# Kernel optimization log

Measured on AMD Instinct MI355X. Metric: run time of the kernel, lower is better.

Reference implementation:

```python
import jax, jax.numpy as jnp
import numpy as np

L, B, C, OUT = 4, 4, 256, 4
H, W = 128, 128
HEADS, DH, G = 8, 32, 64
N = H * W
INNER = HEADS * DH
HID = 4 * C


def _ln(x, w, b, eps=1e-5):
    m = jnp.mean(x, -1, keepdims=True)
    v = jnp.mean((x - m) ** 2, -1, keepdims=True)
    return (x - m) / jnp.sqrt(v + eps) * w + b


def setup_inputs() -> dict:
    key = jax.random.key(0)
    ks = iter(jax.random.split(key, 16))
    nrm = lambda shape, s=0.02: jax.random.normal(next(ks), shape, jnp.float32) * s
    return dict(
        fx=jax.random.normal(next(ks), (B, N, C), jnp.float32),
        ln1_w=jnp.ones((L, C)), ln1_b=jnp.zeros((L, C)),
        convx_w=nrm((L, 3, 3, C, INNER)), convx_b=jnp.zeros((L, INNER)),
        convfx_w=nrm((L, 3, 3, C, INNER)), convfx_b=jnp.zeros((L, INNER)),
        slice_w=nrm((L, DH, G)), slice_b=jnp.zeros((L, G)),
        temperature=0.5 * jnp.ones((L, HEADS)),
        wq=nrm((L, DH, DH)), wk=nrm((L, DH, DH)), wv=nrm((L, DH, DH)),
        wo=nrm((L, INNER, C)), bo=jnp.zeros((L, C)),
        ln2_w=jnp.ones((L, C)), ln2_b=jnp.zeros((L, C)),
        w1=nrm((L, C, HID)), b1=jnp.zeros((L, HID)),
        w2=nrm((L, HID, C)), b2=jnp.zeros((L, C)),
        ln3_w=jnp.ones((C,)), ln3_b=jnp.zeros((C,)),
        w_out=nrm((C, OUT)), b_out=jnp.zeros((OUT,)),
    )


def reference(fx, ln1_w, ln1_b, convx_w, convx_b, convfx_w, convfx_b,
              slice_w, slice_b, temperature, wq, wk, wv, wo, bo,
              ln2_w, ln2_b, w1, b1, w2, b2, ln3_w, ln3_b, w_out, b_out):
    Bb = fx.shape[0]
    scale = DH ** -0.5
    for i in range(L):
        # --- Physics attention (slice attention) ---
        x = _ln(fx, ln1_w[i], ln1_b[i])
        ximg = x.reshape(Bb, H, W, C)  # NHWC
        conv = lambda w, b: jax.lax.conv_general_dilated(
            ximg, w, (1, 1), 'SAME',
            dimension_numbers=('NHWC', 'HWIO', 'NHWC')) + b
        fx_mid = conv(convfx_w[i], convfx_b[i]).reshape(Bb, N, HEADS, DH).transpose(0, 2, 1, 3)  # [B,h,N,d]
        x_mid = conv(convx_w[i], convx_b[i]).reshape(Bb, N, HEADS, DH).transpose(0, 2, 1, 3)
        temp = jnp.clip(temperature[i], 0.1, 5.0)[None, :, None, None]
        logits = (jnp.einsum('bhnd,dg->bhng', x_mid, slice_w[i]) + slice_b[i]) / temp
        sw = jax.nn.softmax(logits, axis=-1)  # [B,h,N,G]
        norm = sw.sum(2)  # [B,h,G]
        st = jnp.einsum('bhnc,bhng->bhgc', fx_mid, sw) / (norm + 1e-5)[..., None]  # [B,h,G,d]
        q = jnp.einsum('bhgc,cd->bhgd', st, wq[i])
        k = jnp.einsum('bhgc,cd->bhgd', st, wk[i])
        v = jnp.einsum('bhgc,cd->bhgd', st, wv[i])
        attn = jax.nn.softmax(jnp.einsum('bhgd,bhkd->bhgk', q, k) * scale, axis=-1)
        ot = jnp.einsum('bhgk,bhkd->bhgd', attn, v)  # [B,h,G,d]
        out_x = jnp.einsum('bhgc,bhng->bhnc', ot, sw)  # deslice back to points
        out_x = out_x.transpose(0, 2, 1, 3).reshape(Bb, N, INNER)
        fx = fx + out_x @ wo[i] + bo[i]
        # --- MLP (n_layers=0, no res inside) ---
        h = _ln(fx, ln2_w[i], ln2_b[i])
        h = jax.nn.gelu(h @ w1[i] + b1[i], approximate=False) @ w2[i] + b2[i]
        fx = fx + h
    # last-layer head
    return _ln(fx, ln3_w, ln3_b) @ w_out + b_out
```

## Files before the change

kernel.cpp:

```cpp
#include <hip/hip_runtime.h>
#include <hip/hip_bf16.h>

typedef __hip_bfloat16 bf16;
typedef __bf16 bfv8 __attribute__((ext_vector_type(8)));
typedef float f32x4 __attribute__((ext_vector_type(4)));

#define BB 4
#define HH 128
#define WWI 128
#define NN 16384
#define CC 256
#define LL 4
#define NHEADS 8
#define DHD 32
#define GG 64
#define INNERC 256
#define HIDD 1024
#define SPLIT 32
#define SSP 16

__device__ __forceinline__ float b2f(bf16 x) { return __bfloat162float(x); }
__device__ __forceinline__ bf16 f2b(float x) { return __float2bfloat16(x); }
__device__ __forceinline__ float us2f(unsigned short v) {
  return __uint_as_float(((unsigned)v) << 16);
}

__device__ __forceinline__ void async16(void* l, const void* g) {
  __builtin_amdgcn_global_load_lds(
      (const __attribute__((address_space(1))) void*)g,
      (__attribute__((address_space(3))) void*)l, 16, 0, 0);
}

__device__ __forceinline__ float wave_sum(float v) {
#pragma unroll
  for (int off = 32; off > 0; off >>= 1) v += __shfl_down(v, off, 64);
  return v;
}

__device__ __forceinline__ float gelu_exact(float x) {
  return 0.5f * x * (1.0f + erff(x * 0.70710678118654752f));
}

__global__ void transpose_cast_kernel(const float* __restrict__ src, bf16* __restrict__ dst,
                                      int R, int Cm) {
  __shared__ float tile[32][33];
  int tb = blockIdx.z;
  const float* s = src + (size_t)tb * R * Cm;
  bf16* d = dst + (size_t)tb * R * Cm;
  int c0 = blockIdx.x * 32, r0 = blockIdx.y * 32;
  int tx = threadIdx.x & 31, ty = threadIdx.x >> 5;
  for (int rr = ty; rr < 32; rr += 8) {
    int r = r0 + rr, c = c0 + tx;
    tile[rr][tx] = (r < R && c < Cm) ? s[(size_t)r * Cm + c] : 0.f;
  }
  __syncthreads();
  for (int cc = ty; cc < 32; cc += 8) {
    int c = c0 + cc, r = r0 + tx;
    if (c < Cm && r < R) d[(size_t)c * R + r] = f2b(tile[tx][cc]);
  }
}

__global__ void ln_kernel(const float* __restrict__ x, const float* __restrict__ w,
                          const float* __restrict__ b, bf16* __restrict__ out) {
  int pp = blockIdx.x;
  int t = threadIdx.x;
  float v = x[(size_t)pp * CC + t];
  float s = wave_sum(v);
  float sq = wave_sum(v * v);
  __shared__ float ls[4], lq[4];
  int wid = t >> 6, lane = t & 63;
  if (lane == 0) { ls[wid] = s; lq[wid] = sq; }
  __syncthreads();
  float tot = ls[0] + ls[1] + ls[2] + ls[3];
  float totq = lq[0] + lq[1] + lq[2] + lq[3];
  float mean = tot * (1.0f / CC);
  float var = totq * (1.0f / CC) - mean * mean;
  float rstd = rsqrtf(var + 1e-5f);
  float o = (v - mean) * rstd * w[t] + b[t];
  out[(size_t)pp * CC + t] = f2b(o);
}

__global__ __launch_bounds__(512) void conv_mfma_kernel(
    const bf16* __restrict__ xln, const bf16* __restrict__ wt,
    const float* __restrict__ bias, bf16* __restrict__ out,
    const float* __restrict__ zbuf) {
  __shared__ __align__(16) unsigned short As[3 * 130 * 64];
  __shared__ __align__(16) unsigned short Bsm[2][256 * 64];
  int bid = blockIdx.x;
  bid = (bid & 7) * 64 + (bid >> 3);
  int h = bid & 127;
  int b = bid >> 7;
  int t = threadIdx.x, lane = t & 63, wid = t >> 6;
  int wm = (wid & 1) * 64, wn = (wid >> 1) * 64;
  int l15 = lane & 15, l4 = lane >> 4;
  int wu = t & ~63;
  f32x4 acc[4][4];
#pragma unroll
  for (int mi = 0; mi < 4; ++mi)
#pragma unroll
    for (int ni = 0; ni < 4; ++ni) acc[mi][ni] = (f32x4){0.f, 0.f, 0.f, 0.f};
  const bf16* xbase = xln + (size_t)b * NN * CC;

  for (int q = 0; q < 4; ++q) {
#pragma unroll
    for (int k = 0; k < 6; ++k) {
      int u = t + k * 512;
      int jp = u & 7, pc = u >> 3;
      int r = pc / 130, cl = pc - r * 130;
      int j = jp ^ (cl & 7);
      int gr = h + r - 1, gc = cl - 1;
      const void* src =
          ((unsigned)gr < 128u && (unsigned)gc < 128u)
              ? (const void*)(xbase + ((size_t)(gr * WWI + gc)) * CC + q * 64 + j * 8)
              : (const void*)zbuf;
      async16(&As[(size_t)(wu + k * 512) * 8], src);
    }
    if (t < 48) {
      int u = t + 3072;
      int jp = u & 7, pc = u >> 3;
      int r = pc / 130, cl = pc - r * 130;
      int j = jp ^ (cl & 7);
      int gr = h + r - 1, gc = cl - 1;
      uint4 v = make_uint4(0u, 0u, 0u, 0u);
      if ((unsigned)gr < 128u && (unsigned)gc < 128u)
        v = *(const uint4*)(xbase + ((size_t)(gr * WWI + gc)) * CC + q * 64 + j * 8);
      *(uint4*)(&As[(size_t)u * 8]) = v;
    }
#pragma unroll
    for (int k = 0; k < 4; ++k) {
      int u = t + k * 512;
      int n = u >> 3, jp = u & 7, j = jp ^ (n & 7);
      async16(&Bsm[0][(size_t)(wu + k * 512) * 8],
              wt + (size_t)n * 256 + q * 64 + j * 8);
    }
    __syncthreads();

    for (int tap = 0; tap < 9; ++tap) {
      int cur = tap & 1;
      if (tap < 8) {
#pragma unroll
        for (int k = 0; k < 4; ++k) {
          int u = t + k * 512;
          int n = u >> 3, jp = u & 7, j = jp ^ (n & 7);
          async16(&Bsm[cur ^ 1][(size_t)(wu + k * 512) * 8],
                  wt + ((size_t)((tap + 1) * 256 + n)) * 256 + q * 64 + j * 8);
        }
      }
      int ky = tap / 3, kx = tap - ky * 3;
      const unsigned short* Bc = Bsm[cur];
#pragma unroll
      for (int s = 0; s < 2; ++s) {
        bfv8 af[4], bfr[4];
#pragma unroll
        for (int mi = 0; mi < 4; ++mi) {
          int cl = wm + mi * 16 + l15 + kx;
          af[mi] = *(const bfv8*)(&As[((size_t)(ky * 130 + cl)) * 64 +
                                      (((s * 4 + l4) ^ (cl & 7)) << 3)]);
        }
#pragma unroll
        for (int ni = 0; ni < 4; ++ni) {
          int rn = wn + ni * 16 + l15;
          bfr[ni] = *(const bfv8*)(&Bc[(size_t)rn * 64 + (((s * 4 + l4) ^ (rn & 7)) << 3)]);
        }
#pragma unroll
        for (int mi = 0; mi < 4; ++mi)
#pragma unroll
          for (int ni = 0; ni < 4; ++ni)
            acc[mi][ni] = __builtin_amdgcn_mfma_f32_16x16x32_bf16(af[mi], bfr[ni], acc[mi][ni], 0, 0, 0);
      }
      __syncthreads();
    }
  }
  int colB = wn + l15;
  int rowB = wm + l4 * 4;
#pragma unroll
  for (int ni = 0; ni < 4; ++ni) {
    int oc = colB + ni * 16;
    float bv = bias[oc];
#pragma unroll
    for (int mi = 0; mi < 4; ++mi) {
#pragma unroll
      for (int r = 0; r < 4; ++r) {
        int pix = rowB + mi * 16 + r;
        out[((size_t)(b * NN + h * WWI + pix)) * CC + oc] = f2b(acc[mi][ni][r] + bv);
      }
    }
  }
}

__global__ __launch_bounds__(256, 2) void gemm_acc_kernel(
    const bf16* __restrict__ A, const bf16* __restrict__ BT,
    const float* __restrict__ bias, float* __restrict__ outf,
    int M, int N, int K, size_t strideAz, size_t strideBz, size_t strideOz) {
  A  += (size_t)blockIdx.z * strideAz;
  BT += (size_t)blockIdx.z * strideBz;
  __shared__ __align__(16) unsigned short As[128 * 64];
  __shared__ __align__(16) unsigned short Bs[128 * 64];
  int m0 = blockIdx.x * 128, n0 = blockIdx.y * 128;
  int t = threadIdx.x, lane = t & 63, wid = t >> 6;
  int wm = (wid >> 1) * 64, wn = (wid & 1) * 64;
  int l15 = lane & 15, q4 = lane >> 4;
  int wg = wm >> 4, ng = wn >> 4;
  f32x4 acc[4][4];
#pragma unroll
  for (int mi = 0; mi < 4; ++mi)
#pragma unroll
    for (int ni = 0; ni < 4; ++ni) acc[mi][ni] = (f32x4){0.f, 0.f, 0.f, 0.f};

  for (int kb = 0; kb < K; kb += 64) {
    __syncthreads();
#pragma unroll
    for (int i = 0; i < 4; ++i) {
      int inst = wid * 4 + i;
      int g = inst >> 1, h2 = inst & 1;
      int row = g * 16 + l15;
      int kc = (h2 * 4 + q4) * 8;
      async16(&As[(size_t)g * 1024 + h2 * 512], A + (size_t)(m0 + row) * K + kb + kc);
      async16(&Bs[(size_t)g * 1024 + h2 * 512], BT + (size_t)(n0 + row) * K + kb + kc);
    }
    __syncthreads();
#pragma unroll
    for (int s = 0; s < 2; ++s) {
      int kgrp = s * 4 + q4;
      bfv8 af[4], bfr[4];
#pragma unroll
      for (int mi = 0; mi < 4; ++mi)
        af[mi] = *(const bfv8*)(&As[(size_t)(wg + mi) * 1024 + kgrp * 128 + l15 * 8]);
#pragma unroll
      for (int ni = 0; ni < 4; ++ni)
        bfr[ni] = *(const bfv8*)(&Bs[(size_t)(ng + ni) * 1024 + kgrp * 128 + l15 * 8]);
#pragma unroll
      for (int mi = 0; mi < 4; ++mi)
#pragma unroll
        for (int ni = 0; ni < 4; ++ni)
          acc[mi][ni] = __builtin_amdgcn_mfma_f32_16x16x32_bf16(af[mi], bfr[ni], acc[mi][ni], 0, 0, 0);
    }
  }
  int colB = n0 + wn + l15;
  int rowB = m0 + wm + q4 * 4;
#pragma unroll
  for (int ni = 0; ni < 4; ++ni) {
    int col = colB + ni * 16;
    float bv = bias[col];
#pragma unroll
    for (int mi = 0; mi < 4; ++mi) {
#pragma unroll
      for (int r = 0; r < 4; ++r) {
        int row = rowB + mi * 16 + r;
        outf[(size_t)blockIdx.z * strideOz + (size_t)row * N + col] += acc[mi][ni][r] + bv;
      }
    }
  }
}

__global__ __launch_bounds__(512) void mlp_fused_kernel(
    const bf16* __restrict__ xln, const bf16* __restrict__ w1t,
    const float* __restrict__ b1, const bf16* __restrict__ w2t,
    const float* __restrict__ b2, float* __restrict__ fx) {
  __shared__ __align__(16) unsigned short As[64 * 256];
  __shared__ __align__(16) bf16 Hs[64 * 128];
  __shared__ __align__(16) unsigned short Wb[128 * 256];
  int m0 = blockIdx.x * 64;
  int t = threadIdx.x, lane = t & 63, wid = t >> 6;
  int l15 = lane & 15, q4 = lane >> 4;
  int wm2 = (wid & 1) * 32, wn2 = (wid >> 1) * 32;
  int wm = (wid & 1) * 32, wn = (wid >> 1) * 64;
  int wu = t & ~63;

  const unsigned short* xg = (const unsigned short*)xln + (size_t)m0 * 256;
#pragma unroll
  for (int i = 0; i < 4; ++i) {
    int u = t + i * 512;
    int row = u >> 5;
    int su = (u & ~7) | ((u & 7) ^ (row & 7));
    async16(&As[(size_t)(wu + i * 512) * 8], xg + (size_t)su * 8);
  }
#pragma unroll
  for (int i = 0; i < 8; ++i) {
    int u = t + i * 512;
    int n = u >> 5, v = u & 31;
    int sv = (v & ~7) | ((v & 7) ^ (n & 7));
    async16(&Wb[(size_t)(wu + i * 512) * 8], w1t + (size_t)n * 256 + sv * 8);
  }

  f32x4 accO[2][4];
#pragma unroll
  for (int mi = 0; mi < 2; ++mi)
#pragma unroll
    for (int ni = 0; ni < 4; ++ni) accO[mi][ni] = (f32x4){0.f, 0.f, 0.f, 0.f};
  __syncthreads();

  for (int j = 0; j < 8; ++j) {
    int hbase = j * 128;
    f32x4 acc2[2][2];
#pragma unroll
    for (int mi = 0; mi < 2; ++mi)
#pragma unroll
      for (int nj = 0; nj < 2; ++nj) acc2[mi][nj] = (f32x4){0.f, 0.f, 0.f, 0.f};
#pragma unroll
    for (int kb = 0; kb < 4; ++kb) {
#pragma unroll
      for (int ks = 0; ks < 2; ++ks) {
        int kgrp = ks * 4 + q4;
        bfv8 af[2], bfr[2];
#pragma unroll
        for (int mi = 0; mi < 2; ++mi) {
          int row = wm2 + mi * 16 + l15;
          af[mi] = *(const bfv8*)(&As[row * 256 + kb * 64 + ((kgrp ^ (row & 7)) << 3)]);
        }
#pragma unroll
        for (int nj = 0; nj < 2; ++nj) {
          int n = wn2 + nj * 16 + l15;
          bfr[nj] = *(const bfv8*)(&Wb[n * 256 + kb * 64 + ((kgrp ^ (n & 7)) << 3)]);
        }
#pragma unroll
        for (int mi = 0; mi < 2; ++mi)
#pragma unroll
          for (int nj = 0; nj < 2; ++nj)
            acc2[mi][nj] = __builtin_amdgcn_mfma_f32_16x16x32_bf16(af[mi], bfr[nj], acc2[mi][nj], 0, 0, 0);
      }
    }
    __syncthreads();
#pragma unroll
    for (int i = 0; i < 8; ++i) {
      int u = t + i * 512;
      int n = u >> 4, v = u & 15;
      int sv = (v & ~7) | ((v & 7) ^ (n & 7));
      async16(&Wb[(size_t)(wu + i * 512) * 8], w2t + (size_t)n * 1024 + hbase + sv * 8);
    }
#pragma unroll
    for (int nj = 0; nj < 2; ++nj) {
      int coln = wn2 + nj * 16 + l15;
      float bv = b1[hbase + coln];
      int half = coln >> 6, sub = (coln >> 3) & 7, lo = coln & 7;
#pragma unroll
      for (int mi = 0; mi < 2; ++mi) {
#pragma unroll
        for (int r = 0; r < 4; ++r) {
          int row = wm2 + mi * 16 + q4 * 4 + r;
          float v = acc2[mi][nj][r] + bv;
          Hs[row * 128 + half * 64 + (((sub ^ (row & 7)) << 3) + lo)] = f2b(gelu_exact(v));
        }
      }
    }
    __syncthreads();
#pragma unroll
    for (int kb2 = 0; kb2 < 2; ++kb2) {
#pragma unroll
      for (int ks = 0; ks < 2; ++ks) {
        int kgrp = ks * 4 + q4;
        bfv8 af[2], bfr[4];
#pragma unroll
        for (int mi = 0; mi < 2; ++mi) {
          int row = wm + mi * 16 + l15;
          af[mi] = *(const bfv8*)(&Hs[row * 128 + kb2 * 64 + ((kgrp ^ (row & 7)) << 3)]);
        }
#pragma unroll
        for (int ni = 0; ni < 4; ++ni) {
          int n = wn + ni * 16 + l15;
          bfr[ni] = *(const bfv8*)(&Wb[n * 128 + kb2 * 64 + ((kgrp ^ (n & 7)) << 3)]);
        }
#pragma unroll
        for (int mi = 0; mi < 2; ++mi)
#pragma unroll
          for (int ni = 0; ni < 4; ++ni)
            accO[mi][ni] = __builtin_amdgcn_mfma_f32_16x16x32_bf16(af[mi], bfr[ni], accO[mi][ni], 0, 0, 0);
      }
    }
    if (j < 7) {
      __syncthreads();
#pragma unroll
      for (int i = 0; i < 8; ++i) {
        int u = t + i * 512;
        int n = u >> 5, v = u & 31;
        int sv = (v & ~7) | ((v & 7) ^ (n & 7));
        async16(&Wb[(size_t)(wu + i * 512) * 8],
                w1t + (size_t)(hbase + 128 + n) * 256 + sv * 8);
      }
      __syncthreads();
    }
  }
#pragma unroll
  for (int ni = 0; ni < 4; ++ni) {
    int col = wn + ni * 16 + l15;
    float bv = b2[col];
#pragma unroll
    for (int mi = 0; mi < 2; ++mi) {
#pragma unroll
      for (int r = 0; r < 4; ++r) {
        int row = m0 + wm + mi * 16 + q4 * 4 + r;
        fx[(size_t)row * 256 + col] += accO[mi][ni][r] + bv;
      }
    }
  }
}

__global__ __launch_bounds__(256) void slice_softmax_kernel(
    const bf16* __restrict__ xmid, const float* __restrict__ sw_w,
    const float* __restrict__ sw_b, const float* __restrict__ temp,
    bf16* __restrict__ swout) {
  __shared__ float wsm[32][64];
  __shared__ float xm[SSP][256];
  __shared__ float bias_s[64];
  __shared__ float rtc[8];
  int p0 = blockIdx.x * SSP;
  int t = threadIdx.x;
  for (int i = t; i < 2048; i += 256) wsm[i >> 6][i & 63] = sw_w[i];
  if (t < 64) bias_s[t] = sw_b[t];
  if (t < 8) {
    float x = temp[t];
    rtc[t] = 1.0f / fminf(fmaxf(x, 0.1f), 5.0f);
  }
  const unsigned short* xg = (const unsigned short*)xmid + (size_t)p0 * 256;
#pragma unroll
  for (int i2 = t; i2 < SSP * 32; i2 += 256) {
    uint4 v = ((const uint4*)xg)[i2];
    int p = i2 >> 5, c = (i2 & 31) << 3;
    xm[p][c + 0] = us2f((unsigned short)(v.x & 0xffff));
    xm[p][c + 1] = us2f((unsigned short)(v.x >> 16));
    xm[p][c + 2] = us2f((unsigned short)(v.y & 0xffff));
    xm[p][c + 3] = us2f((unsigned short)(v.y >> 16));
    xm[p][c + 4] = us2f((unsigned short)(v.z & 0xffff));
    xm[p][c + 5] = us2f((unsigned short)(v.z >> 16));
    xm[p][c + 6] = us2f((unsigned short)(v.w & 0xffff));
    xm[p][c + 7] = us2f((unsigned short)(v.w >> 16));
  }
  __syncthreads();
  int g = t & 63, pq = t >> 6;
  for (int pp2 = 0; pp2 < SSP / 4; ++pp2) {
    int p = pp2 * 4 + pq;
#pragma unroll
    for (int h = 0; h < NHEADS; ++h) {
      float acc = bias_s[g];
      const float* xr = &xm[p][h * 32];
#pragma unroll
      for (int d = 0; d < 32; ++d) acc += xr[d] * wsm[d][g];
      float logit = acc * rtc[h];
      float m = logit;
#pragma unroll
      for (int off = 32; off > 0; off >>= 1) m = fmaxf(m, __shfl_xor(m, off, 64));
      float e = __expf(logit - m);
      float s = e;
#pragma unroll
      for (int off = 32; off > 0; off >>= 1) s += __shfl_xor(s, off, 64);
      swout[(size_t)(p0 + p) * 512 + h * 64 + g] = f2b(e / s);
    }
  }
}

__global__ __launch_bounds__(256) void slice_st_kernel(
    const bf16* __restrict__ fxmid, const bf16* __restrict__ sw,
    float* __restrict__ stp, float* __restrict__ normp) {
  __shared__ __align__(16) unsigned short sw_s[64 * 64];
  __shared__ __align__(16) unsigned short fx_s[32 * 64];
  __shared__ float npart[2][64];
  int split = blockIdx.x, h = blockIdx.y, b = blockIdx.z;
  int t = threadIdx.x, w = t >> 6, lane = t & 63;
  int l15 = lane & 15, q4 = lane >> 4;
  int ns0 = split * (NN / SPLIT);
  const int NT = (NN / SPLIT) / 64;
  f32x4 acc0 = {0.f, 0.f, 0.f, 0.f}, acc1 = {0.f, 0.f, 0.f, 0.f};
  float nacc = 0.f;
  const unsigned short* swg = (const unsigned short*)sw + (size_t)b * NN * 512 + h * 64;
  const unsigned short* fxg = (const unsigned short*)fxmid + (size_t)b * NN * 256 + h * 32;

  for (int kt = 0; kt < NT; ++kt) {
    int n0 = ns0 + kt * 64;
    __syncthreads();
    if (w < 2) {
      int g = lane;
#pragma unroll
      for (int i = 0; i < 4; ++i) {
        int j = w + 2 * i;
        const unsigned short* p = swg + (size_t)(n0 + j * 8) * 512 + g;
        unsigned short v0 = p[0],     v1 = p[512],  v2 = p[1024], v3 = p[1536];
        unsigned short v4 = p[2048],  v5 = p[2560], v6 = p[3072], v7 = p[3584];
        nacc += us2f(v0) + us2f(v1) + us2f(v2) + us2f(v3) +
                us2f(v4) + us2f(v5) + us2f(v6) + us2f(v7);
        uint4 pk = make_uint4((unsigned)v0 | ((unsigned)v1 << 16),
                              (unsigned)v2 | ((unsigned)v3 << 16),
                              (unsigned)v4 | ((unsigned)v5 << 16),
                              (unsigned)v6 | ((unsigned)v7 << 16));
        ((uint4*)sw_s)[g * 8 + (j ^ (g & 7))] = pk;
      }
    } else {
      int d = lane & 31, nh = lane >> 5, w3 = w - 2;
#pragma unroll
      for (int i = 0; i < 2; ++i) {
        int nbase = (w3 * 2 + i) * 16 + nh * 8;
        const unsigned short* p = fxg + (size_t)(n0 + nbase) * 256 + d;
        unsigned short v0 = p[0],    v1 = p[256],  v2 = p[512],  v3 = p[768];
        unsigned short v4 = p[1024], v5 = p[1280], v6 = p[1536], v7 = p[1792];
        uint4 pk = make_uint4((unsigned)v0 | ((unsigned)v1 << 16),
                              (unsigned)v2 | ((unsigned)v3 << 16),
                              (unsigned)v4 | ((unsigned)v5 << 16),
                              (unsigned)v6 | ((unsigned)v7 << 16));
        int u = nbase >> 3;
        ((uint4*)fx_s)[d * 8 + (u ^ (d & 7))] = pk;
      }
    }
    __syncthreads();
    int gg = w * 16 + l15;
    int d0 = l15, d1 = 16 + l15;
#pragma unroll
    for (int ks = 0; ks < 2; ++ks) {
      bfv8 af  = ((const bfv8*)sw_s)[gg * 8 + ((ks * 4 + q4) ^ (gg & 7))];
      bfv8 bf0 = ((const bfv8*)fx_s)[d0 * 8 + ((ks * 4 + q4) ^ (d0 & 7))];
      bfv8 bf1 = ((const bfv8*)fx_s)[d1 * 8 + ((ks * 4 + q4) ^ (d1 & 7))];
      acc0 = __builtin_amdgcn_mfma_f32_16x16x32_bf16(af, bf0, acc0, 0, 0, 0);
      acc1 = __builtin_amdgcn_mfma_f32_16x16x32_bf16(af, bf1, acc1, 0, 0, 0);
    }
  }
  if (w < 2) npart[w][lane] = nacc;
  __syncthreads();
  int bh = b * NHEADS + h;
  if (t < 64) normp[(size_t)split * (BB * NHEADS * GG) + bh * 64 + t] = npart[0][t] + npart[1][t];
  size_t base = ((size_t)split * (BB * NHEADS * GG) + bh * 64) * 32;
#pragma unroll
  for (int r = 0; r < 4; ++r) {
    int g = w * 16 + q4 * 4 + r;
    stp[base + (size_t)g * 32 + l15] = acc0[r];
    stp[base + (size_t)g * 32 + 16 + l15] = acc1[r];
  }
}

__global__ __launch_bounds__(256) void attn_kernel(
    const float* __restrict__ stp, const float* __restrict__ normp,
    const float* __restrict__ wq, const float* __restrict__ wk,
    const float* __restrict__ wv, float* __restrict__ ot) {
  __shared__ float wqs[32 * 32], wks[32 * 32], wvs[32 * 32];
  __shared__ float st[GG][DHD + 1];
  __shared__ float qq[GG][DHD + 1], kk[GG][DHD + 1], vv[GG][DHD + 1];
  __shared__ float pm[GG][GG + 1];
  __shared__ float nrm[GG];
  int bh = blockIdx.x;
  int t = threadIdx.x;
  ((float4*)wqs)[t] = ((const float4*)wq)[t];
  ((float4*)wks)[t] = ((const float4*)wk)[t];
  ((float4*)wvs)[t] = ((const float4*)wv)[t];
  if (t < 64) {
    float ns = 0.f;
    for (int s = 0; s < SPLIT; ++s) ns += normp[(size_t)s * (BB * NHEADS * GG) + bh * 64 + t];
    nrm[t] = 1.0f / (ns + 1e-5f);
  }
  __syncthreads();
#pragma unroll
  for (int i = 0; i < 8; ++i) {
    int idx = t + i * 256;
    int g = idx >> 5, d = idx & 31;
    float a = 0.f;
    for (int s = 0; s < SPLIT; ++s)
      a += stp[((size_t)s * (BB * NHEADS * GG) + bh * 64 + g) * 32 + d];
    st[g][d] = a * nrm[g];
  }
  __syncthreads();
#pragma unroll
  for (int i = 0; i < 8; ++i) {
    int idx = t + i * 256;
    int g = idx >> 5, d = idx & 31;
    float aq = 0.f, ak = 0.f, av = 0.f;
#pragma unroll
    for (int c = 0; c < 32; ++c) {
      float sv = st[g][c];
      aq += sv * wqs[c * 32 + d];
      ak += sv * wks[c * 32 + d];
      av += sv * wvs[c * 32 + d];
    }
    qq[g][d] = aq; kk[g][d] = ak; vv[g][d] = av;
  }
  __syncthreads();
  {
    int g = t >> 2, sub = t & 3;
    float sc[16];
    float m = -1e30f;
    const float scale = 0.17677669529663687f;
#pragma unroll
    for (int jj = 0; jj < 16; ++jj) {
      int j = sub * 16 + jj;
      float a = 0.f;
#pragma unroll
      for (int d = 0; d < 32; ++d) a += qq[g][d] * kk[j][d];
      a *= scale;
      sc[jj] = a;
      m = fmaxf(m, a);
    }
    m = fmaxf(m, __shfl_xor(m, 1, 64));
    m = fmaxf(m, __shfl_xor(m, 2, 64));
    float ssum = 0.f;
#pragma unroll
    for (int jj = 0; jj < 16; ++jj) { sc[jj] = __expf(sc[jj] - m); ssum += sc[jj]; }
    ssum += __shfl_xor(ssum, 1, 64);
    ssum += __shfl_xor(ssum, 2, 64);
    float rs = 1.0f / ssum;
#pragma unroll
    for (int jj = 0; jj < 16; ++jj) pm[g][sub * 16 + jj] = sc[jj] * rs;
  }
  __syncthreads();
#pragma unroll
  for (int i = 0; i < 8; ++i) {
    int idx = t + i * 256;
    int g = idx >> 5, d = idx & 31;
    float a = 0.f;
#pragma unroll
    for (int j = 0; j < GG; ++j) a += pm[g][j] * vv[j][d];
    ot[((size_t)bh * GG + g) * DHD + d] = a;
  }
}

__global__ __launch_bounds__(256) void wc_kernel(const float* __restrict__ ot,
                                                 const float* __restrict__ wo,
                                                 bf16* __restrict__ wct) {
  __shared__ float ots[GG][DHD];
  int bh = blockIdx.x;
  int h = bh & 7, b = bh >> 3;
  int t = threadIdx.x;
  for (int i = t; i < GG * DHD; i += 256) ots[i >> 5][i & 31] = ot[(size_t)bh * (GG * DHD) + i];
  float wol[DHD];
#pragma unroll
  for (int d = 0; d < DHD; ++d) wol[d] = wo[(size_t)(h * DHD + d) * CC + t];
  __syncthreads();
  bf16* dst = wct + ((size_t)b * CC + t) * (NHEADS * GG) + h * GG;
#pragma unroll 4
  for (int g = 0; g < GG; ++g) {
    float a = 0.f;
#pragma unroll
    for (int d = 0; d < DHD; ++d) a += wol[d] * ots[g][d];
    dst[g] = f2b(a);
  }
}

__global__ void head_kernel(const float* __restrict__ fx, const float* __restrict__ w,
                            const float* __restrict__ b, const float* __restrict__ wout,
                            const float* __restrict__ bout, float* __restrict__ out) {
  int pp = blockIdx.x;
  int t = threadIdx.x;
  float v = fx[(size_t)pp * CC + t];
  float s = wave_sum(v);
  float sq = wave_sum(v * v);
  __shared__ float ls[4], lq[4];
  int wid = t >> 6, lane = t & 63;
  if (lane == 0) { ls[wid] = s; lq[wid] = sq; }
  __syncthreads();
  float tot = ls[0] + ls[1] + ls[2] + ls[3];
  float totq = lq[0] + lq[1] + lq[2] + lq[3];
  float mean = tot * (1.0f / CC);
  float var = totq * (1.0f / CC) - mean * mean;
  float rstd = rsqrtf(var + 1e-5f);
  float xn = (v - mean) * rstd * w[t] + b[t];
  __shared__ float xs[CC];
  xs[t] = xn;
  __syncthreads();
  if (t < 4) {
    float a = bout[t];
    for (int c = 0; c < CC; ++c) a += xs[c] * wout[c * 4 + t];
    out[(size_t)pp * 4 + t] = a;
  }
}

extern "C" void kernel_launch(void* const* d_in, const int* in_sizes, int n_in,
                              void* d_out, int out_size, void* d_ws, size_t ws_size,
                              hipStream_t stream) {
  const float* fx_in      = (const float*)d_in[0];
  const float* ln1_w      = (const float*)d_in[1];
  const float* ln1_b      = (const float*)d_in[2];
  const float* convx_w    = (const float*)d_in[3];
  const float* convx_b    = (const float*)d_in[4];
  const float* convfx_w   = (const float*)d_in[5];
  const float* convfx_b   = (const float*)d_in[6];
  const float* slice_w    = (const float*)d_in[7];
  const float* slice_b    = (const float*)d_in[8];
  const float* temperature= (const float*)d_in[9];
  const float* wq         = (const float*)d_in[10];
  const float* wk         = (const float*)d_in[11];
  const float* wv         = (const float*)d_in[12];
  const float* wo         = (const float*)d_in[13];
  const float* bo         = (const float*)d_in[14];
  const float* ln2_w      = (const float*)d_in[15];
  const float* ln2_b      = (const float*)d_in[16];
  const float* w1         = (const float*)d_in[17];
  const float* b1         = (const float*)d_in[18];
  const float* w2         = (const float*)d_in[19];
  const float* b2         = (const float*)d_in[20];
  const float* ln3_w      = (const float*)d_in[21];
  const float* ln3_b      = (const float*)d_in[22];
  const float* w_out      = (const float*)d_in[23];
  const float* b_out      = (const float*)d_in[24];
  float* out = (float*)d_out;

  char* ws = (char*)d_ws;
  size_t off = 0;
  auto alloc = [&](size_t bytes) -> void* {
    void* p = ws + off;
    off += (bytes + 255) & ~(size_t)255;
    return p;
  };
  float* fx32  = (float*)alloc((size_t)BB * NN * CC * 4);
  bf16* xln    = (bf16*)alloc((size_t)BB * NN * CC * 2);
  char* uni    = (char*)alloc((size_t)BB * NN * 512 * 2 * 2);
  bf16* xmid   = (bf16*)uni;
  bf16* fxmid  = (bf16*)(uni + (size_t)BB * NN * INNERC * 2);
  bf16* swb    = (bf16*)(uni + (size_t)2 * BB * NN * INNERC * 2);
  float* stp   = (float*)uni;
  float* normp = (float*)(uni + (size_t)SPLIT * BB * NHEADS * GG * DHD * 4);
  bf16* wtx    = (bf16*)alloc((size_t)LL * 9 * CC * INNERC * 2);
  bf16* wtfx   = (bf16*)alloc((size_t)LL * 9 * CC * INNERC * 2);
  bf16* w1t    = (bf16*)alloc((size_t)LL * CC * HIDD * 2);
  bf16* w2t    = (bf16*)alloc((size_t)LL * HIDD * CC * 2);
  float* otb   = (float*)alloc((size_t)BB * NHEADS * GG * DHD * 4);
  bf16* wct    = (bf16*)alloc((size_t)BB * CC * NHEADS * GG * 2);
  float* zbuf  = (float*)alloc(256);
  (void)ws_size; (void)in_sizes; (void)n_in; (void)out_size;

  hipMemsetAsync(zbuf, 0, 256, stream);

  transpose_cast_kernel<<<dim3(8, 8, LL * 9), 256, 0, stream>>>(convx_w, wtx, CC, INNERC);
  transpose_cast_kernel<<<dim3(8, 8, LL * 9), 256, 0, stream>>>(convfx_w, wtfx, CC, INNERC);
  transpose_cast_kernel<<<dim3(32, 8, LL), 256, 0, stream>>>(w1, w1t, CC, HIDD);
  transpose_cast_kernel<<<dim3(8, 32, LL), 256, 0, stream>>>(w2, w2t, HIDD, CC);

  hipMemcpyAsync(fx32, fx_in, (size_t)BB * NN * CC * sizeof(float),
                 hipMemcpyDeviceToDevice, stream);

  const int M = BB * NN;
  for (int i = 0; i < LL; ++i) {
    ln_kernel<<<M, 256, 0, stream>>>(fx32, ln1_w + i * CC, ln1_b + i * CC, xln);
    conv_mfma_kernel<<<BB * HH, 512, 0, stream>>>(
        xln, wtfx + (size_t)i * 9 * CC * INNERC, convfx_b + i * INNERC, fxmid,
        (const float*)zbuf);
    conv_mfma_kernel<<<BB * HH, 512, 0, stream>>>(
        xln, wtx + (size_t)i * 9 * CC * INNERC, convx_b + i * INNERC, xmid,
        (const float*)zbuf);
    slice_softmax_kernel<<<M / SSP, 256, 0, stream>>>(
        xmid, slice_w + i * DHD * GG, slice_b + i * GG, temperature + i * NHEADS, swb);
    slice_st_kernel<<<dim3(SPLIT, NHEADS, BB), 256, 0, stream>>>(fxmid, swb, stp, normp);
    attn_kernel<<<BB * NHEADS, 256, 0, stream>>>(
        stp, normp, wq + i * DHD * DHD, wk + i * DHD * DHD, wv + i * DHD * DHD, otb);
    wc_kernel<<<BB * NHEADS, 256, 0, stream>>>(otb, wo + (size_t)i * INNERC * CC, wct);
    gemm_acc_kernel<<<dim3(NN / 128, CC / 128, BB), 256, 0, stream>>>(
        swb, wct, bo + i * CC, fx32, NN, CC, NHEADS * GG,
        (size_t)NN * (NHEADS * GG), (size_t)CC * (NHEADS * GG), (size_t)NN * CC);
    ln_kernel<<<M, 256, 0, stream>>>(fx32, ln2_w + i * CC, ln2_b + i * CC, xln);
    mlp_fused_kernel<<<M / 64, 512, 0, stream>>>(
        xln, w1t + (size_t)i * CC * HIDD, b1 + i * HIDD,
        w2t + (size_t)i * HIDD * CC, b2 + i * CC, fx32);
  }
  head_kernel<<<M, 256, 0, stream>>>(fx32, ln3_w, ln3_b, w_out, b_out, out);
}
```

Measured before the change: 2.763 ms.

## Double-buffer MLP weight tiles in small chunks and parallelize head projection

The fused MLP kernel now stages W1 and W2 in small 16KB chunks into a two-slot shared buffer, prefetching the next chunk while MFMAs run on the current one. This replaces one large 64KB weight buffer that was loaded with a stall before each phase. The smaller LDS footprint plus a launch-bounds occupancy hint lets more blocks reside per CU. The final head kernel now computes its 4 outputs with all four waves using wave reductions instead of 4 serial threads. The change costs one extra barrier per k-chunk, and the new unswizzled weight layout may cause LDS bank conflicts.

After: 2.924 ms. 5.8% more time.

```diff
diff --git a/kernel.cpp b/kernel.cpp
--- a/kernel.cpp
+++ b/kernel.cpp
@@ -253,13 +253,13 @@
   }
 }
 
-__global__ __launch_bounds__(512) void mlp_fused_kernel(
+__global__ __launch_bounds__(512, 4) void mlp_fused_kernel(
     const bf16* __restrict__ xln, const bf16* __restrict__ w1t,
     const float* __restrict__ b1, const bf16* __restrict__ w2t,
     const float* __restrict__ b2, float* __restrict__ fx) {
   __shared__ __align__(16) unsigned short As[64 * 256];
   __shared__ __align__(16) bf16 Hs[64 * 128];
-  __shared__ __align__(16) unsigned short Wb[128 * 256];
+  __shared__ __align__(16) unsigned short Wb[2][1024 * 8];
   int m0 = blockIdx.x * 64;
   int t = threadIdx.x, lane = t & 63, wid = t >> 6;
   int l15 = lane & 15, q4 = lane >> 4;
@@ -267,6 +267,25 @@
   int wm = (wid & 1) * 32, wn = (wid >> 1) * 64;
   int wu = t & ~63;
 
+  auto stageW1 = [&](int buf, int hb, int kb) {
+#pragma unroll
+    for (int i = 0; i < 2; ++i) {
+      int u = t + i * 512;
+      int n = u & 127, kg = u >> 7;
+      async16(&Wb[buf][(size_t)(wu + i * 512) * 8],
+              w1t + (size_t)(hb + n) * 256 + kb * 64 + kg * 8);
+    }
+  };
+  auto stageW2 = [&](int buf, int hb, int kc) {
+#pragma unroll
+    for (int i = 0; i < 2; ++i) {
+      int u = t + i * 512;
+      int n = u & 255, kg = u >> 8;
+      async16(&Wb[buf][(size_t)(wu + i * 512) * 8],
+              w2t + (size_t)n * 1024 + hb + kc * 32 + kg * 8);
+    }
+  };
+
   const unsigned short* xg = (const unsigned short*)xln + (size_t)m0 * 256;
 #pragma unroll
   for (int i = 0; i < 4; ++i) {
@@ -275,13 +294,7 @@
     int su = (u & ~7) | ((u & 7) ^ (row & 7));
     async16(&As[(size_t)(wu + i * 512) * 8], xg + (size_t)su * 8);
   }
-#pragma unroll
-  for (int i = 0; i < 8; ++i) {
-    int u = t + i * 512;
-    int n = u >> 5, v = u & 31;
-    int sv = (v & ~7) | ((v & 7) ^ (n & 7));
-    async16(&Wb[(size_t)(wu + i * 512) * 8], w1t + (size_t)n * 256 + sv * 8);
-  }
+  stageW1(0, 0, 0);
 
   f32x4 accO[2][4];
 #pragma unroll
@@ -299,6 +312,9 @@
       for (int nj = 0; nj < 2; ++nj) acc2[mi][nj] = (f32x4){0.f, 0.f, 0.f, 0.f};
 #pragma unroll
     for (int kb = 0; kb < 4; ++kb) {
+      if (kb < 3) stageW1((kb & 1) ^ 1, hbase, kb + 1);
+      else        stageW2(0, hbase, 0);
+      const unsigned short* Wh = Wb[kb & 1];
 #pragma unroll
       for (int ks = 0; ks < 2; ++ks) {
         int kgrp = ks * 4 + q4;
@@ -311,7 +327,7 @@
 #pragma unroll
         for (int nj = 0; nj < 2; ++nj) {
           int n = wn2 + nj * 16 + l15;
-          bfr[nj] = *(const bfv8*)(&Wb[n * 256 + kb * 64 + ((kgrp ^ (n & 7)) << 3)]);
+          bfr[nj] = ((const bfv8*)Wh)[kgrp * 128 + n];
         }
 #pragma unroll
         for (int mi = 0; mi < 2; ++mi)
@@ -319,15 +335,9 @@
           for (int nj = 0; nj < 2; ++nj)
             acc2[mi][nj] = __builtin_amdgcn_mfma_f32_16x16x32_bf16(af[mi], bfr[nj], acc2[mi][nj], 0, 0, 0);
       }
-    }
-    __syncthreads();
-#pragma unroll
-    for (int i = 0; i < 8; ++i) {
-      int u = t + i * 512;
-      int n = u >> 4, v = u & 15;
-      int sv = (v & ~7) | ((v & 7) ^ (n & 7));
-      async16(&Wb[(size_t)(wu + i * 512) * 8], w2t + (size_t)n * 1024 + hbase + sv * 8);
-    }
+      __syncthreads();
+    }
+    stageW2(1, hbase, 1);
 #pragma unroll
     for (int nj = 0; nj < 2; ++nj) {
       int coln = wn2 + nj * 16 + l15;
@@ -345,38 +355,27 @@
     }
     __syncthreads();
 #pragma unroll
-    for (int kb2 = 0; kb2 < 2; ++kb2) {
-#pragma unroll
-      for (int ks = 0; ks < 2; ++ks) {
-        int kgrp = ks * 4 + q4;
-        bfv8 af[2], bfr[4];
-#pragma unroll
-        for (int mi = 0; mi < 2; ++mi) {
-          int row = wm + mi * 16 + l15;
-          af[mi] = *(const bfv8*)(&Hs[row * 128 + kb2 * 64 + ((kgrp ^ (row & 7)) << 3)]);
-        }
-#pragma unroll
-        for (int ni = 0; ni < 4; ++ni) {
-          int n = wn + ni * 16 + l15;
-          bfr[ni] = *(const bfv8*)(&Wb[n * 128 + kb2 * 64 + ((kgrp ^ (n & 7)) << 3)]);
-        }
-#pragma unroll
-        for (int mi = 0; mi < 2; ++mi)
-#pragma unroll
-          for (int ni = 0; ni < 4; ++ni)
-            accO[mi][ni] = __builtin_amdgcn_mfma_f32_16x16x32_bf16(af[mi], bfr[ni], accO[mi][ni], 0, 0, 0);
-      }
-    }
-    if (j < 7) {
-      __syncthreads();
-#pragma unroll
-      for (int i = 0; i < 8; ++i) {
-        int u = t + i * 512;
-        int n = u >> 5, v = u & 31;
-        int sv = (v & ~7) | ((v & 7) ^ (n & 7));
-        async16(&Wb[(size_t)(wu + i * 512) * 8],
-                w1t + (size_t)(hbase + 128 + n) * 256 + sv * 8);
-      }
+    for (int kc = 0; kc < 4; ++kc) {
+      if (kc == 1 || kc == 2) stageW2((kc & 1) ^ 1, hbase, kc + 1);
+      else if (kc == 3 && j < 7) stageW1(0, hbase + 128, 0);
+      const unsigned short* Wh = Wb[kc & 1];
+      bfv8 af[2], bfr[4];
+#pragma unroll
+      for (int mi = 0; mi < 2; ++mi) {
+        int row = wm + mi * 16 + l15;
+        af[mi] = *(const bfv8*)(&Hs[row * 128 + (kc >> 1) * 64 +
+                                    ((((kc & 1) * 4 + q4) ^ (row & 7)) << 3)]);
+      }
+#pragma unroll
+      for (int ni = 0; ni < 4; ++ni) {
+        int n = wn + ni * 16 + l15;
+        bfr[ni] = ((const bfv8*)Wh)[q4 * 256 + n];
+      }
+#pragma unroll
+      for (int mi = 0; mi < 2; ++mi)
+#pragma unroll
+        for (int ni = 0; ni < 4; ++ni)
+          accO[mi][ni] = __builtin_amdgcn_mfma_f32_16x16x32_bf16(af[mi], bfr[ni], accO[mi][ni], 0, 0, 0);
       __syncthreads();
     }
   }
@@ -650,11 +649,11 @@
   __shared__ float xs[CC];
   xs[t] = xn;
   __syncthreads();
-  if (t < 4) {
-    float a = bout[t];
-    for (int c = 0; c < CC; ++c) a += xs[c] * wout[c * 4 + t];
-    out[(size_t)pp * 4 + t] = a;
-  }
+  float a = 0.f;
+#pragma unroll
+  for (int c0 = 0; c0 < CC; c0 += 64) a += xs[c0 + lane] * wout[(c0 + lane) * 4 + wid];
+  a = wave_sum(a);
+  if (lane == 0) out[(size_t)pp * 4 + wid] = a + bout[wid];
 }
 
 extern "C" void kernel_launch(void* const* d_in, const int* in_sizes, int n_in,
```
